# Optimization experiments

Hardware: AMD Instinct MI355X
Metric: run time of the kernel (lower is better)

Reference implementation:

```python
import jax, jax.numpy as jnp
from jax import lax
import numpy as np

B, T, H31, W = 16, 96, 31, 64
C1, C2, LH, NC = 16, 32, 64, 10

def _conv(x, w, b):
    # NCHW conv, 3x3, padding=1 ('SAME'), fused bias + relu
    y = lax.conv_general_dilated(x, w, (1, 1), 'SAME', dimension_numbers=('NCHW', 'OIHW', 'NCHW'))
    return jax.nn.relu(y + b[None, :, None, None])

def _lstm(xs, w_ih, w_hh, b):
    # xs: [T, B, D]; PyTorch gate order i, f, g, o
    Hd = w_hh.shape[1]
    def step(carry, x):
        h, c = carry
        g = x @ w_ih.T + h @ w_hh.T + b
        i, f, gg, o = jnp.split(g, 4, -1)
        c = jax.nn.sigmoid(f) * c + jax.nn.sigmoid(i) * jnp.tanh(gg)
        h = jax.nn.sigmoid(o) * jnp.tanh(c)
        return (h, c), h
    z = jnp.zeros((xs.shape[1], Hd), xs.dtype)
    _, hs = lax.scan(step, (z, z), xs)
    return hs  # [T, B, H]

def setup_inputs():
    key = jax.random.key(0)
    ks = jax.random.split(key, 26)
    n = lambda i, shape, s=0.1: jax.random.normal(ks[i], shape, jnp.float32) * s
    return {
        'x_real': jax.random.normal(ks[0], (B, T, H31, W), jnp.float32),
        'x_imag': jax.random.normal(ks[1], (B, T, H31, W), jnp.float32),
        'lengths': jax.random.randint(ks[2], (B,), 1, T + 1),
        'conv1r_w': n(3, (C1, 1, 3, 3), 0.3), 'conv1r_b': n(4, (C1,)),
        'conv1i_w': n(5, (C1, 1, 3, 3), 0.3), 'conv1i_b': n(6, (C1,)),
        'conv2r_w': n(7, (C2, C1, 3, 3), 0.15), 'conv2r_b': n(8, (C2,)),
        'conv2i_w': n(9, (C2, C1, 3, 3), 0.15), 'conv2i_b': n(10, (C2,)),
        'fus_w': n(11, (2 * C2, 4 * C2), 0.1), 'fus_b': n(12, (2 * C2,)),
        'wf_ih': n(13, (4 * LH, 2 * C2), 0.1), 'wf_hh': n(14, (4 * LH, LH), 0.1),
        'bf_ih': n(15, (4 * LH,)), 'bf_hh': n(16, (4 * LH,)),
        'wb_ih': n(17, (4 * LH, 2 * C2), 0.1), 'wb_hh': n(18, (4 * LH, LH), 0.1),
        'bb_ih': n(19, (4 * LH,)), 'bb_hh': n(20, (4 * LH,)),
        'fc_w': n(21, (NC, 2 * LH), 0.1), 'fc_b': n(22, (NC,)),
    }

def reference(x_real, x_imag, lengths, conv1r_w, conv1r_b, conv1i_w, conv1i_b, conv2r_w, conv2r_b, conv2i_w, conv2i_b, fus_w, fus_b, wf_ih, wf_hh, bf_ih, bf_hh, wb_ih, wb_hh, bb_ih, bb_hh, fc_w, fc_b):
    Bb, Tt, Hh, Ww = x_real.shape
    # batch all (sample, timestep) conv work together: [B*T, 1, 31, W]
    xr = x_real.reshape(Bb * Tt, 1, Hh, Ww)
    xi = x_imag.reshape(Bb * Tt, 1, Hh, Ww)
    rf = _conv(_conv(xr, conv1r_w, conv1r_b), conv2r_w, conv2r_b)
    mf = _conv(_conv(xi, conv1i_w, conv1i_b), conv2i_w, conv2i_b)
    r = rf.mean((-2, -1))  # AdaptiveAvgPool2d((1,1)) -> [B*T, C2]
    m = mf.mean((-2, -1))
    mag = jnp.sqrt(r * r + m * m)           # abs(r + 1j*m)
    ang = jnp.arctan2(m, r)                 # angle(r + 1j*m)
    feat = jnp.concatenate([r, m, mag, ang], -1)  # [B*T, 4*C2]
    fused = jax.nn.relu(feat @ fus_w.T + fus_b).reshape(Bb, Tt, -1)  # dropout = identity (eval)
    # forward LSTM: output at t < length is unaffected by padded steps
    hs_f = _lstm(fused.transpose(1, 0, 2), wf_ih, wf_hh, bf_ih + bf_hh)  # [T, B, LH]
    last_f = hs_f[lengths - 1, jnp.arange(Bb)]
    # backward LSTM over length-reversed sequence (packed-sequence semantics)
    rev_idx = jnp.clip(lengths[:, None] - 1 - jnp.arange(Tt)[None, :], 0, Tt - 1)  # [B, T]
    x_rev = jnp.take_along_axis(fused, rev_idx[:, :, None], axis=1)
    hs_b = _lstm(x_rev.transpose(1, 0, 2), wb_ih, wb_hh, bb_ih + bb_hh)
    # backward hidden at original position length-1 is the first reverse step
    last = jnp.concatenate([last_f, hs_b[0]], -1)  # [B, 2*LH]
    return last @ fc_w.T + fc_b
```

## Files before the change

kernel.cpp:

```cpp
#include <hip/hip_runtime.h>
#include <math.h>

#define BB 16
#define TT 96
#define HH 31
#define WW 64
#define BT (BB*TT)
#define C1 16
#define C2 32
#define LH 64
#define NC 10

typedef _Float16 half8 __attribute__((ext_vector_type(8)));
typedef float floatx16 __attribute__((ext_vector_type(16)));

#define XPAD 66
#define YPAD 33
#define NPOS (YPAD*XPAD)
#define SXBYTES (NPOS*32 + 128)

__device__ __forceinline__ int swz(int byte) {
    return byte ^ (((byte >> 7) & 7) << 4);
}

__global__ __launch_bounds__(512, 2)
void conv_pool_mfma(const float* __restrict__ xr, const float* __restrict__ xi,
                    const float* __restrict__ w1r, const float* __restrict__ b1r,
                    const float* __restrict__ w1i, const float* __restrict__ b1i,
                    const float* __restrict__ w2r, const float* __restrict__ b2r,
                    const float* __restrict__ w2i, const float* __restrict__ b2i,
                    float* __restrict__ pool_r, float* __restrict__ pool_m)
{
    __shared__ __align__(128) unsigned char s_x[SXBYTES];
    __shared__ float s_pool[C2];

    const int tid  = threadIdx.x;
    const int lane = tid & 63;
    const int img  = blockIdx.x;
    const int part = blockIdx.y;

    const float* xg = (part ? xi : xr) + img*(HH*WW);
    const float* w1 = part ? w1i : w1r;
    const float* b1 = part ? b1i : b1r;
    const float* w2 = part ? w2i : w2r;
    const float* b2 = part ? b2i : b2r;
    float* poolo = (part ? pool_m : pool_r) + img*C2;

    if (tid < C2) s_pool[tid] = 0.f;

    if (tid < 194) {
        int pos;
        if (tid < 66)       pos = tid;
        else if (tid < 132) pos = 32*XPAD + (tid - 66);
        else {
            int i = tid - 132;
            pos = (1 + (i >> 1))*XPAD + ((i & 1) ? 65 : 0);
        }
        *reinterpret_cast<int4*>(s_x + swz(pos*32))      = make_int4(0,0,0,0);
        *reinterpret_cast<int4*>(s_x + swz(pos*32 + 16)) = make_int4(0,0,0,0);
    }

    if (tid < HH*16) {
        const int y  = tid >> 4;
        const int x0 = (tid & 15) << 2;
        float patch[3][6];
        #pragma unroll
        for (int ky = 0; ky < 3; ++ky) {
            int row = y + ky - 1;
            #pragma unroll
            for (int j = 0; j < 6; ++j) {
                int col = x0 + j - 1;
                patch[ky][j] = (row >= 0 && row < HH && col >= 0 && col < WW)
                                 ? xg[row*WW + col] : 0.f;
            }
        }
        #pragma unroll
        for (int p = 0; p < 2; ++p) {
            float acc[8][4];
            #pragma unroll
            for (int ch = 0; ch < 8; ++ch) {
                float bb = b1[p*8 + ch];
                #pragma unroll
                for (int j = 0; j < 4; ++j) acc[ch][j] = bb;
            }
            #pragma unroll
            for (int ky = 0; ky < 3; ++ky)
                #pragma unroll
                for (int kx = 0; kx < 3; ++kx) {
                    #pragma unroll
                    for (int ch = 0; ch < 8; ++ch) {
                        float wv = w1[(p*8 + ch)*9 + ky*3 + kx];
                        #pragma unroll
                        for (int j = 0; j < 4; ++j)
                            acc[ch][j] += patch[ky][kx + j] * wv;
                    }
                }
            #pragma unroll
            for (int j = 0; j < 4; ++j) {
                half8 v;
                #pragma unroll
                for (int ch = 0; ch < 8; ++ch)
                    v[ch] = (_Float16)fmaxf(acc[ch][j], 0.f);
                int pos = (y + 1)*XPAD + (x0 + j + 1);
                *reinterpret_cast<half8*>(s_x + swz(pos*32 + p*16)) = v;
            }
        }
    }

    const int oc  = lane & 31;
    const int icb = (lane >> 5) * 8;
    half8 af[9];
    #pragma unroll
    for (int t = 0; t < 9; ++t) {
        half8 v;
        #pragma unroll
        for (int i = 0; i < 8; ++i)
            v[i] = (_Float16)w2[(oc*C1 + icb + i)*9 + t];
        af[t] = v;
    }
    float bias[16];
    #pragma unroll
    for (int r = 0; r < 16; ++r)
        bias[r] = b2[(r & 3) + 8*(r >> 2) + 4*(lane >> 5)];

    __syncthreads();

    float pool[16];
    #pragma unroll
    for (int r = 0; r < 16; ++r) pool[r] = 0.f;

    const int wav = tid >> 6;
    const int halfoff = (lane >> 5) << 4;

    #define LDB(dst, ky, kx) do { \
        int byte_ = (pbase + (ky)*XPAD + (kx))*32 + halfoff; \
        dst = *reinterpret_cast<const half8*>(s_x + swz(byte_)); } while (0)

    for (int tile = wav; tile < 62; tile += 8) {
        int y  = tile >> 1;
        int x0 = (tile & 1) * 32;
        int pbase = y*XPAD + x0 + (lane & 31);
        floatx16 acc;
        #pragma unroll
        for (int r = 0; r < 16; ++r) acc[r] = bias[r];

        half8 r0a, r0b, r0c, r1a, r1b, r1c, r2a, r2b, r2c;
        LDB(r0a, 0, 0); LDB(r0b, 0, 1); LDB(r0c, 0, 2);
        LDB(r1a, 1, 0); LDB(r1b, 1, 1); LDB(r1c, 1, 2);
        acc = __builtin_amdgcn_mfma_f32_32x32x16_f16(af[0], r0a, acc, 0, 0, 0);
        acc = __builtin_amdgcn_mfma_f32_32x32x16_f16(af[1], r0b, acc, 0, 0, 0);
        acc = __builtin_amdgcn_mfma_f32_32x32x16_f16(af[2], r0c, acc, 0, 0, 0);
        LDB(r2a, 2, 0); LDB(r2b, 2, 1); LDB(r2c, 2, 2);
        acc = __builtin_amdgcn_mfma_f32_32x32x16_f16(af[3], r1a, acc, 0, 0, 0);
        acc = __builtin_amdgcn_mfma_f32_32x32x16_f16(af[4], r1b, acc, 0, 0, 0);
        acc = __builtin_amdgcn_mfma_f32_32x32x16_f16(af[5], r1c, acc, 0, 0, 0);
        acc = __builtin_amdgcn_mfma_f32_32x32x16_f16(af[6], r2a, acc, 0, 0, 0);
        acc = __builtin_amdgcn_mfma_f32_32x32x16_f16(af[7], r2b, acc, 0, 0, 0);
        acc = __builtin_amdgcn_mfma_f32_32x32x16_f16(af[8], r2c, acc, 0, 0, 0);

        #pragma unroll
        for (int r = 0; r < 16; ++r) pool[r] += fmaxf(acc[r], 0.f);
    }
    #undef LDB

    #pragma unroll
    for (int m = 1; m <= 16; m <<= 1) {
        #pragma unroll
        for (int r = 0; r < 16; ++r) pool[r] += __shfl_xor(pool[r], m, 64);
    }
    if ((lane & 31) == 0) {
        #pragma unroll
        for (int r = 0; r < 16; ++r)
            atomicAdd(&s_pool[(r & 3) + 8*(r >> 2) + 4*(lane >> 5)], pool[r]);
    }
    __syncthreads();
    if (tid < C2) poolo[tid] = s_pool[tid] * (1.f/1984.f);
}

__device__ __forceinline__ float sigm(float x){ return 1.f/(1.f + __expf(-x)); }
__device__ __forceinline__ float ftanh(float x){
    float xc = fminf(fmaxf(x, -15.f), 15.f);
    float e = __expf(2.f*xc);
    return (e - 1.f)/(e + 1.f);
}

__global__ __launch_bounds__(256)
void lstm_prep(const float* __restrict__ pool_r, const float* __restrict__ pool_m,
               const float* __restrict__ fus_w, const float* __restrict__ fus_b,
               const float* __restrict__ wf_ih,
               const float* __restrict__ bf_ih, const float* __restrict__ bf_hh,
               float* __restrict__ fusedg, float* __restrict__ gates_x)
{
    __shared__ __align__(16) float s_feat[128];
    __shared__ __align__(16) float s_fused[64];
    const int bt  = blockIdx.x;
    const int tid = threadIdx.x;

    if (tid < 32) {
        float r = pool_r[bt*C2 + tid];
        float m = pool_m[bt*C2 + tid];
        s_feat[tid]      = r;
        s_feat[32 + tid] = m;
        s_feat[64 + tid] = sqrtf(r*r + m*m);
        s_feat[96 + tid] = atan2f(m, r);
    }
    __syncthreads();

    if (tid < 64) {
        float acc = fus_b[tid];
        const float4* wv = reinterpret_cast<const float4*>(fus_w + tid*128);
        float a0=0.f, a1=0.f, a2=0.f, a3=0.f;
        #pragma unroll
        for (int q = 0; q < 32; ++q) {
            float4 w = wv[q];
            float4 f = *reinterpret_cast<const float4*>(s_feat + q*4);
            a0 += w.x*f.x; a1 += w.y*f.y; a2 += w.z*f.z; a3 += w.w*f.w;
        }
        float v = fmaxf(acc + (a0+a1) + (a2+a3), 0.f);
        s_fused[tid] = v;
        fusedg[bt*64 + tid] = v;
    }
    __syncthreads();

    {
        float acc = bf_ih[tid] + bf_hh[tid];
        const float4* wv = reinterpret_cast<const float4*>(wf_ih + tid*64);
        float a0=0.f, a1=0.f, a2=0.f, a3=0.f;
        #pragma unroll
        for (int q = 0; q < 16; ++q) {
            float4 w = wv[q];
            float4 f = *reinterpret_cast<const float4*>(s_fused + q*4);
            a0 += w.x*f.x; a1 += w.y*f.y; a2 += w.z*f.z; a3 += w.w*f.w;
        }
        gates_x[bt*256 + tid] = acc + (a0+a1) + (a2+a3);
    }
}

__global__ __launch_bounds__(256, 1)
void lstm_scan(const float* __restrict__ gates_x, const float* __restrict__ fusedg,
               const int* __restrict__ lengths,
               const float* __restrict__ wf_hh,
               const float* __restrict__ wb_ih,
               const float* __restrict__ bb_ih, const float* __restrict__ bb_hh,
               float* __restrict__ last_f, float* __restrict__ hb0)
{
    const int tid = threadIdx.x;
    const int b   = blockIdx.x & 15;
    const int len = lengths[b];

    if (blockIdx.x < 16) {
        __shared__ __align__(16) float s_h[2][64];
        const int ln = tid & 63;
        const int w  = tid >> 6;
        const int q  = ln >> 4;
        const int u  = w*16 + (ln & 15);
        const int g  = q*64 + u;

        float whh[64];
        #pragma unroll
        for (int j = 0; j < 64; j += 4) {
            float4 a = *reinterpret_cast<const float4*>(wf_hh + g*64 + j);
            whh[j]=a.x; whh[j+1]=a.y; whh[j+2]=a.z; whh[j+3]=a.w;
        }
        if (q == 0) s_h[0][u] = 0.f;
        __syncthreads();

        const float* gxp = gates_x + (b*TT)*256 + g;
        float gx = gxp[0];
        float creg = 0.f;
        for (int t = 0; t < TT; ++t) {
            float gxn = (t+1 < TT) ? gxp[(t+1)*256] : 0.f;

            const int cur = t & 1;
            float a0=0.f, a1=0.f, a2=0.f, a3=0.f;
            #pragma unroll
            for (int j = 0; j < 64; j += 4) {
                float4 hv = *reinterpret_cast<const float4*>(&s_h[cur][j]);
                a0 += whh[j]*hv.x;   a1 += whh[j+1]*hv.y;
                a2 += whh[j+2]*hv.z; a3 += whh[j+3]*hv.w;
            }
            float acc = gx + (a0+a1) + (a2+a3);

            float p1 = __shfl_xor(acc, 16, 64);
            float p2 = __shfl_xor(acc, 32, 64);
            float p3 = __shfl_xor(p1,  32, 64);
            float g0 = (q==0)?acc : (q==1)?p1 : (q==2)?p2 : p3;
            float g1 = (q==1)?acc : (q==0)?p1 : (q==3)?p2 : p3;
            float g2 = (q==2)?acc : (q==3)?p1 : (q==0)?p2 : p3;
            float g3 = (q==3)?acc : (q==2)?p1 : (q==1)?p2 : p3;

            creg = sigm(g1)*creg + sigm(g0)*ftanh(g2);
            float h = sigm(g3)*ftanh(creg);

            if (q == 0) {
                s_h[cur^1][u] = h;
                if (t == len-1) last_f[b*64 + u] = h;
            }
            gx = gxn;
            __syncthreads();
        }
    } else {
        __shared__ __align__(16) float s_f[64];
        __shared__ float s_g[256];
        if (tid < 64) s_f[tid] = fusedg[(b*TT + (len-1))*64 + tid];
        __syncthreads();
        {
            float acc = bb_ih[tid] + bb_hh[tid];
            const float4* wv = reinterpret_cast<const float4*>(wb_ih + tid*64);
            float a0=0.f, a1=0.f, a2=0.f, a3=0.f;
            #pragma unroll
            for (int qq = 0; qq < 16; ++qq) {
                float4 wvv = wv[qq];
                float4 f = *reinterpret_cast<const float4*>(s_f + qq*4);
                a0 += wvv.x*f.x; a1 += wvv.y*f.y; a2 += wvv.z*f.z; a3 += wvv.w*f.w;
            }
            s_g[tid] = acc + (a0+a1) + (a2+a3);
        }
        __syncthreads();
        if (tid < 64) {
            float iv = sigm(s_g[tid]);
            float gv = ftanh(s_g[128+tid]);
            float ov = sigm(s_g[192+tid]);
            hb0[b*64 + tid] = ov*ftanh(iv*gv);
        }
    }
}

__global__ __launch_bounds__(256)
void final_fc_kernel(const float* __restrict__ last_f, const float* __restrict__ hb0,
                     const float* __restrict__ fc_w, const float* __restrict__ fc_b,
                     float* __restrict__ out)
{
    int t = threadIdx.x;
    if (t >= BB*NC) return;
    int b = t / NC, k = t % NC;
    float acc = fc_b[k];
    const float* w = fc_w + k*128;
    #pragma unroll
    for (int j = 0; j < 64; ++j) acc += last_f[b*64+j]*w[j];
    #pragma unroll
    for (int j = 0; j < 64; ++j) acc += hb0[b*64+j]*w[64+j];
    out[b*NC + k] = acc;
}

extern "C" void kernel_launch(void* const* d_in, const int* in_sizes, int n_in,
                              void* d_out, int out_size, void* d_ws, size_t ws_size,
                              hipStream_t stream)
{
    const float* x_real = (const float*)d_in[0];
    const float* x_imag = (const float*)d_in[1];
    const int*   lengths= (const int*)d_in[2];
    const float* c1r_w = (const float*)d_in[3];
    const float* c1r_b = (const float*)d_in[4];
    const float* c1i_w = (const float*)d_in[5];
    const float* c1i_b = (const float*)d_in[6];
    const float* c2r_w = (const float*)d_in[7];
    const float* c2r_b = (const float*)d_in[8];
    const float* c2i_w = (const float*)d_in[9];
    const float* c2i_b = (const float*)d_in[10];
    const float* fus_w = (const float*)d_in[11];
    const float* fus_b = (const float*)d_in[12];
    const float* wf_ih = (const float*)d_in[13];
    const float* wf_hh = (const float*)d_in[14];
    const float* bf_ih = (const float*)d_in[15];
    const float* bf_hh = (const float*)d_in[16];
    const float* wb_ih = (const float*)d_in[17];
    const float* wb_hh = (const float*)d_in[18];
    const float* bb_ih = (const float*)d_in[19];
    const float* bb_hh = (const float*)d_in[20];
    const float* fc_w  = (const float*)d_in[21];
    const float* fc_b  = (const float*)d_in[22];
    float* out = (float*)d_out;

    float* ws      = (float*)d_ws;
    float* pool_r  = ws;
    float* pool_m  = pool_r  + BT*C2;
    float* fusedg  = pool_m  + BT*C2;
    float* gates_x = fusedg  + BT*64;
    float* last_f  = gates_x + BT*256;
    float* hb0     = last_f  + BB*LH;

    conv_pool_mfma<<<dim3(BT, 2), 512, 0, stream>>>(
        x_real, x_imag, c1r_w, c1r_b, c1i_w, c1i_b,
        c2r_w, c2r_b, c2i_w, c2i_b, pool_r, pool_m);

    lstm_prep<<<BT, 256, 0, stream>>>(pool_r, pool_m, fus_w, fus_b,
                                      wf_ih, bf_ih, bf_hh, fusedg, gates_x);

    lstm_scan<<<32, 256, 0, stream>>>(gates_x, fusedg, lengths, wf_hh,
                                      wb_ih, bb_ih, bb_hh, last_f, hb0);

    final_fc_kernel<<<1, 256, 0, stream>>>(last_f, hb0, fc_w, fc_b, out);
}
```

Measured before the change: 299.3 us.

## Split conv image into two row halves per block with partial pools

The fused conv1+conv2+pool kernel now launches a third grid dimension that splits each image into top and bottom row halves. Each block recomputes the conv1 halo row, so its shared tile shrinks from 33 to 18 padded rows. Each half writes an unnormalized partial pool, and lstm_prep sums the two halves and applies the mean scale. The smaller LDS footprint and raised launch bound target higher occupancy and more blocks, at the cost of a duplicated halo row of conv1 work and extra partial-pool traffic.

Result: slower. 595.8 us (+99.0%).

```diff
diff --git a/kernel.cpp b/kernel.cpp
--- a/kernel.cpp
+++ b/kernel.cpp
@@ -15,94 +15,98 @@
 typedef float floatx16 __attribute__((ext_vector_type(16)));
 
 #define XPAD 66
-#define YPAD 33
-#define NPOS (YPAD*XPAD)
-#define SXBYTES (NPOS*32 + 128)
+#define LROWS 18
+#define SXB2 (LROWS*XPAD*32 + 128)
 
 __device__ __forceinline__ int swz(int byte) {
     return byte ^ (((byte >> 7) & 7) << 4);
 }
 
-__global__ __launch_bounds__(512, 2)
+__global__ __launch_bounds__(512, 8)
 void conv_pool_mfma(const float* __restrict__ xr, const float* __restrict__ xi,
                     const float* __restrict__ w1r, const float* __restrict__ b1r,
                     const float* __restrict__ w1i, const float* __restrict__ b1i,
                     const float* __restrict__ w2r, const float* __restrict__ b2r,
                     const float* __restrict__ w2i, const float* __restrict__ b2i,
-                    float* __restrict__ pool_r, float* __restrict__ pool_m)
-{
-    __shared__ __align__(128) unsigned char s_x[SXBYTES];
+                    float* __restrict__ poolp_r, float* __restrict__ poolp_m)
+{
+    __shared__ __align__(128) unsigned char s_x[SXB2];
     __shared__ float s_pool[C2];
 
     const int tid  = threadIdx.x;
     const int lane = tid & 63;
     const int img  = blockIdx.x;
     const int part = blockIdx.y;
+    const int hf   = blockIdx.z;
 
     const float* xg = (part ? xi : xr) + img*(HH*WW);
     const float* w1 = part ? w1i : w1r;
     const float* b1 = part ? b1i : b1r;
     const float* w2 = part ? w2i : w2r;
     const float* b2 = part ? b2i : b2r;
-    float* poolo = (part ? pool_m : pool_r) + img*C2;
+    float* poolo = (part ? poolp_m : poolp_r) + (hf*BT + img)*C2;
 
     if (tid < C2) s_pool[tid] = 0.f;
 
-    if (tid < 194) {
+    if (tid < 102) {
         int pos;
-        if (tid < 66)       pos = tid;
-        else if (tid < 132) pos = 32*XPAD + (tid - 66);
+        if (tid < 66) pos = (hf ? 16 : 0)*XPAD + tid;
         else {
-            int i = tid - 132;
-            pos = (1 + (i >> 1))*XPAD + ((i & 1) ? 65 : 0);
+            int i = tid - 66;
+            pos = (i >> 1)*XPAD + ((i & 1) ? 65 : 0);
         }
         *reinterpret_cast<int4*>(s_x + swz(pos*32))      = make_int4(0,0,0,0);
         *reinterpret_cast<int4*>(s_x + swz(pos*32 + 16)) = make_int4(0,0,0,0);
     }
 
-    if (tid < HH*16) {
-        const int y  = tid >> 4;
-        const int x0 = (tid & 15) << 2;
-        float patch[3][6];
-        #pragma unroll
-        for (int ky = 0; ky < 3; ++ky) {
-            int row = y + ky - 1;
+    {
+        const int nr = hf ? 16 : 17;
+        if (tid < nr*16) {
+            const int ry = tid >> 4;
+            const int y  = hf ? (15 + ry) : ry;
+            const int lr = hf ? ry : (ry + 1);
+            const int x0 = (tid & 15) << 2;
+            float patch[3][6];
             #pragma unroll
-            for (int j = 0; j < 6; ++j) {
-                int col = x0 + j - 1;
-                patch[ky][j] = (row >= 0 && row < HH && col >= 0 && col < WW)
-                                 ? xg[row*WW + col] : 0.f;
-            }
-        }
-        #pragma unroll
-        for (int p = 0; p < 2; ++p) {
-            float acc[8][4];
+            for (int ky = 0; ky < 3; ++ky) {
+                int row = y + ky - 1;
+                #pragma unroll
+                for (int j = 0; j < 6; ++j) {
+                    int col = x0 + j - 1;
+                    patch[ky][j] = (row >= 0 && row < HH && col >= 0 && col < WW)
+                                     ? xg[row*WW + col] : 0.f;
+                }
+            }
             #pragma unroll
-            for (int ch = 0; ch < 8; ++ch) {
-                float bb = b1[p*8 + ch];
+            for (int p = 0; p < 2; ++p) {
+                float acc[8][4];
                 #pragma unroll
-                for (int j = 0; j < 4; ++j) acc[ch][j] = bb;
-            }
-            #pragma unroll
-            for (int ky = 0; ky < 3; ++ky)
+                for (int ch = 0; ch < 8; ++ch) {
+                    float bb = b1[p*8 + ch];
+                    #pragma unroll
+                    for (int j = 0; j < 4; ++j) acc[ch][j] = bb;
+                }
                 #pragma unroll
-                for (int kx = 0; kx < 3; ++kx) {
+                for (int ky = 0; ky < 3; ++ky)
                     #pragma unroll
-                    for (int ch = 0; ch < 8; ++ch) {
-                        float wv = w1[(p*8 + ch)*9 + ky*3 + kx];
+                    for (int kx = 0; kx < 3; ++kx) {
                         #pragma unroll
-                        for (int j = 0; j < 4; ++j)
-                            acc[ch][j] += patch[ky][kx + j] * wv;
+                        for (int ch = 0; ch < 8; ++ch) {
+                            float wv = w1[(p*8 + ch)*9 + ky*3 + kx];
+                            #pragma unroll
+                            for (int j = 0; j < 4; ++j)
+                                acc[ch][j] += patch[ky][kx + j] * wv;
+                        }
                     }
+                #pragma unroll
+                for (int j = 0; j < 4; ++j) {
+                    half8 v;
+                    #pragma unroll
+                    for (int ch = 0; ch < 8; ++ch)
+                        v[ch] = (_Float16)fmaxf(acc[ch][j], 0.f);
+                    int pos = lr*XPAD + (x0 + j + 1);
+                    *reinterpret_cast<half8*>(s_x + swz(pos*32 + p*16)) = v;
                 }
-            #pragma unroll
-            for (int j = 0; j < 4; ++j) {
-                half8 v;
-                #pragma unroll
-                for (int ch = 0; ch < 8; ++ch)
-                    v[ch] = (_Float16)fmaxf(acc[ch][j], 0.f);
-                int pos = (y + 1)*XPAD + (x0 + j + 1);
-                *reinterpret_cast<half8*>(s_x + swz(pos*32 + p*16)) = v;
             }
         }
     }
@@ -131,15 +135,16 @@
 
     const int wav = tid >> 6;
     const int halfoff = (lane >> 5) << 4;
+    const int ntiles = hf ? 30 : 32;
 
     #define LDB(dst, ky, kx) do { \
         int byte_ = (pbase + (ky)*XPAD + (kx))*32 + halfoff; \
         dst = *reinterpret_cast<const half8*>(s_x + swz(byte_)); } while (0)
 
-    for (int tile = wav; tile < 62; tile += 8) {
-        int y  = tile >> 1;
+    for (int tile = wav; tile < ntiles; tile += 8) {
+        int ty = tile >> 1;
         int x0 = (tile & 1) * 32;
-        int pbase = y*XPAD + x0 + (lane & 31);
+        int pbase = ty*XPAD + x0 + (lane & 31);
         floatx16 acc;
         #pragma unroll
         for (int r = 0; r < 16; ++r) acc[r] = bias[r];
@@ -174,7 +179,7 @@
             atomicAdd(&s_pool[(r & 3) + 8*(r >> 2) + 4*(lane >> 5)], pool[r]);
     }
     __syncthreads();
-    if (tid < C2) poolo[tid] = s_pool[tid] * (1.f/1984.f);
+    if (tid < C2) poolo[tid] = s_pool[tid];
 }
 
 __device__ __forceinline__ float sigm(float x){ return 1.f/(1.f + __expf(-x)); }
@@ -185,7 +190,7 @@
 }
 
 __global__ __launch_bounds__(256)
-void lstm_prep(const float* __restrict__ pool_r, const float* __restrict__ pool_m,
+void lstm_prep(const float* __restrict__ poolp_r, const float* __restrict__ poolp_m,
                const float* __restrict__ fus_w, const float* __restrict__ fus_b,
                const float* __restrict__ wf_ih,
                const float* __restrict__ bf_ih, const float* __restrict__ bf_hh,
@@ -197,8 +202,8 @@
     const int tid = threadIdx.x;
 
     if (tid < 32) {
-        float r = pool_r[bt*C2 + tid];
-        float m = pool_m[bt*C2 + tid];
+        float r = (poolp_r[bt*C2 + tid] + poolp_r[(BT + bt)*C2 + tid]) * (1.f/1984.f);
+        float m = (poolp_m[bt*C2 + tid] + poolp_m[(BT + bt)*C2 + tid]) * (1.f/1984.f);
         s_feat[tid]      = r;
         s_feat[32 + tid] = m;
         s_feat[64 + tid] = sqrtf(r*r + m*m);
@@ -373,18 +378,18 @@
     float* out = (float*)d_out;
 
     float* ws      = (float*)d_ws;
-    float* pool_r  = ws;
-    float* pool_m  = pool_r  + BT*C2;
-    float* fusedg  = pool_m  + BT*C2;
+    float* poolp_r = ws;
+    float* poolp_m = poolp_r + 2*BT*C2;
+    float* fusedg  = poolp_m + 2*BT*C2;
     float* gates_x = fusedg  + BT*64;
     float* last_f  = gates_x + BT*256;
     float* hb0     = last_f  + BB*LH;
 
-    conv_pool_mfma<<<dim3(BT, 2), 512, 0, stream>>>(
+    conv_pool_mfma<<<dim3(BT, 2, 2), 512, 0, stream>>>(
         x_real, x_imag, c1r_w, c1r_b, c1i_w, c1i_b,
-        c2r_w, c2r_b, c2i_w, c2i_b, pool_r, pool_m);
-
-    lstm_prep<<<BT, 256, 0, stream>>>(pool_r, pool_m, fus_w, fus_b,
+        c2r_w, c2r_b, c2i_w, c2i_b, poolp_r, poolp_m);
+
+    lstm_prep<<<BT, 256, 0, stream>>>(poolp_r, poolp_m, fus_w, fus_b,
                                       wf_ih, bf_ih, bf_hh, fusedg, gates_x);
 
     lstm_scan<<<32, 256, 0, stream>>>(gates_x, fusedg, lengths, wf_hh,
```
